# Performance work log

Hardware: AMD Instinct MI355X
Metric: run time of the kernel (lower is better)

The kernel has to match this reference:

```python
import jax, jax.numpy as jnp
import numpy as np

IN_DIM = 128
OUT_DIM = 128
GRID_SIZE = 10
SPLINE_ORDER = 3  # k
N_TOKENS = 65536
LN_EPS = 1e-5


def setup_inputs() -> dict:
    key = jax.random.key(0)
    k0, k1, k2 = jax.random.split(key, 3)
    x = jax.random.normal(k0, (N_TOKENS, IN_DIM), dtype=jnp.float32)
    # uniform extended grid on [-1, 1]: [in, grid_size + 2k + 1]
    h = 2.0 / GRID_SIZE
    g1d = jnp.arange(-SPLINE_ORDER, GRID_SIZE + SPLINE_ORDER + 1, dtype=jnp.float32) * h - 1.0
    grid = jnp.tile(g1d[None, :], (IN_DIM, 1))
    base_w = jax.random.normal(k1, (OUT_DIM, IN_DIM), dtype=jnp.float32) / np.float32(np.sqrt(IN_DIM))
    n_coeff = GRID_SIZE + SPLINE_ORDER  # basis functions per input dim
    spline_w = jax.random.normal(k2, (OUT_DIM, IN_DIM * n_coeff), dtype=jnp.float32) * np.float32(0.1 / np.sqrt(IN_DIM))
    gamma = jnp.ones((OUT_DIM,), dtype=jnp.float32)
    beta = jnp.zeros((OUT_DIM,), dtype=jnp.float32)
    return {"x": x, "grid": grid, "base_w": base_w, "spline_w": spline_w, "gamma": gamma, "beta": beta}


def _b_splines(x, grid, k=SPLINE_ORDER):
    # x: [N, in], grid: [in, G+2k+1] -> basis [N, in, G+k] via Cox-de Boor
    xe = x[:, :, None]
    b = ((xe >= grid[:, :-1]) & (xe < grid[:, 1:])).astype(x.dtype)  # order-0
    for p in range(1, k + 1):
        left = (xe - grid[:, : -(p + 1)]) / (grid[:, p:-1] - grid[:, : -(p + 1)]) * b[..., :-1]
        right = (grid[:, p + 1 :] - xe) / (grid[:, p + 1 :] - grid[:, 1:-p]) * b[..., 1:]
        b = left + right
    return b


def reference(x, grid, base_w, spline_w, gamma, beta):
    n = x.shape[0]
    basis = _b_splines(x, grid)  # [N, in, G+k]
    kan = jax.nn.silu(x) @ base_w.T + basis.reshape(n, -1) @ spline_w.T  # [N, out]
    # LayerNorm over last dim
    mu = jnp.mean(kan, axis=-1, keepdims=True)
    var = jnp.mean(jnp.square(kan - mu), axis=-1, keepdims=True)
    out = (kan - mu) * jax.lax.rsqrt(var + LN_EPS) * gamma + beta
    # dropout is identity in eval mode; skip = Identity since in_dim == out_dim
    return out + x
```

## Files before the change

kernel.cpp:

```cpp
#include <hip/hip_runtime.h>


#define DIM 128
#define NCOEFF 13
#define SLOT 16
#define KTOT (DIM * SLOT)
#define DPC 8
#define KC (DPC * SLOT)
#define NCHUNK (DIM / DPC)
#define MTILE 64
#define ABUF (MTILE * DPC * SLOT)
#define XSTR 68
#define WB_BYTES (DIM * KTOT * 2)

typedef __attribute__((ext_vector_type(8))) short short8;
typedef __attribute__((ext_vector_type(8))) __bf16 bf16x8;
typedef __attribute__((ext_vector_type(4))) float f32x4;
typedef __attribute__((ext_vector_type(2))) unsigned long long u64x2;

__device__ __forceinline__ unsigned short f2bf(float f) {
  unsigned int u = __builtin_bit_cast(unsigned int, f);
  u += 0x7fffu + ((u >> 16) & 1u);
  return (unsigned short)(u >> 16);
}

__global__ void kan_prep_wfrag(const float* __restrict__ base_w,
                               const float* __restrict__ spline_w,
                               unsigned short* __restrict__ Wf) {
  int u = blockIdx.x * 256 + threadIdx.x;
  int lane = u & 63;
  int blk = u >> 6;
  int ntile = blk & 7;
  int khi = blk >> 3;
  int q = lane >> 4, ln = lane & 15;
  int n = ntile * 16 + ln;
  int k0 = khi * 32 + q * 8;
  unsigned short v[8];
#pragma unroll
  for (int j = 0; j < 8; ++j) {
    int k = k0 + j;
    int i = k >> 4, s = k & 15;
    float f = (s == 0) ? base_w[n * DIM + i]
            : (s <= 13 ? spline_w[n * (DIM * NCOEFF) + i * NCOEFF + (s - 1)] : 0.f);
    v[j] = f2bf(f);
  }
  short8 pack;
#pragma unroll
  for (int j = 0; j < 8; ++j) pack[j] = (short)v[j];
  ((short8*)Wf)[u] = pack;
}

__device__ __forceinline__ void build_slots(float xv, unsigned long long r[4]) {
  float sil = xv * __builtin_amdgcn_rcpf(1.0f + __expf(-xv));
  float tp = (xv + 1.6f) * 5.0f;
  int m = (int)floorf(tp);
  bool valid = (xv >= -1.6f) && (xv < 1.6f);
  m = m < 0 ? 0 : (m > 15 ? 15 : m);
  float u = tp - (float)m;
  float omu = 1.0f - u;
  float w0 = 0.166666667f * omu * omu * omu;
  float w3 = 0.166666667f * u * u * u;
  float w1 = (0.5f * u - 1.0f) * u * u + 0.666666667f;
  float w2 = (0.5f * omu - 1.0f) * omu * omu + 0.666666667f;
  unsigned long long W =
      (unsigned long long)f2bf(w0) |
      ((unsigned long long)f2bf(w1) << 16) |
      ((unsigned long long)f2bf(w2) << 32) |
      ((unsigned long long)f2bf(w3) << 48);
  if (!valid) W = 0;
  int p = m - 2;
#pragma unroll
  for (int j = 0; j < 4; ++j) {
    int d = 64 * j - 16 * p;
    unsigned long long rj;
    if (d >= 64 || d <= -64) rj = 0;
    else if (d >= 0) rj = W >> d;
    else rj = W << (-d);
    r[j] = rj;
  }
  r[0] = (r[0] & ~0xFFFFULL) | (unsigned long long)f2bf(sil);
  r[3] &= 0xFFFFFFFFULL;
}

__device__ __forceinline__ int a_off(int t, int i, int h) {
  return (((i >> 1) * 4 + (t >> 4)) << 9) + ((((i & 1) * 2 + h) << 4) + (t & 15)) * 8;
}

__device__ __forceinline__ void stage_elem(unsigned short* Ab, int t, int i, float xv) {
  unsigned long long r[4];
  build_slots(xv, r);
  *(short8*)(Ab + a_off(t, i, 0)) = __builtin_bit_cast(short8, (u64x2){r[0], r[1]});
  *(short8*)(Ab + a_off(t, i, 1)) = __builtin_bit_cast(short8, (u64x2){r[2], r[3]});
}

template <bool BF16W>
__global__ __launch_bounds__(256, 4)
void kan_fused(const float* __restrict__ x,
               const unsigned short* __restrict__ Wf,
               const float* __restrict__ base_w,
               const float* __restrict__ spline_w,
               const float* __restrict__ gamma,
               const float* __restrict__ beta,
               float* __restrict__ out) {
  __shared__ __align__(16) unsigned short A_lds[2][ABUF];
  __shared__ float x_lds[2][DPC * XSTR];
  __shared__ float S1p[4][MTILE];
  __shared__ float S2p[4][MTILE];

  const int tid = threadIdx.x;
  const int lane = tid & 63, wave = tid >> 6;
  const int q = lane >> 4, ln = lane & 15;
  const long tokBase = (long)blockIdx.x * MTILE;

  f32x4 acc[4][2];
#pragma unroll
  for (int a = 0; a < 4; ++a)
#pragma unroll
    for (int b = 0; b < 2; ++b) acc[a][b] = (f32x4){0.f, 0.f, 0.f, 0.f};

  const int iw = tid & 7;
  const int t0 = tid >> 3;
  const int ts = tid & 63;
  const int i2 = tid >> 6;

  {
    float xa = x[(tokBase + ts) * DIM + i2];
    float xb = x[(tokBase + ts) * DIM + i2 + 4];
    stage_elem(A_lds[0], ts, i2, xa);
    stage_elem(A_lds[0], ts, i2 + 4, xb);
    float f0 = x[(tokBase + t0) * DIM + DPC + iw];
    float f1 = x[(tokBase + t0 + 32) * DIM + DPC + iw];
    x_lds[1][iw * XSTR + t0] = f0;
    x_lds[1][iw * XSTR + t0 + 32] = f1;
  }
  short8 bfr[4][2];
#pragma unroll
  for (int ks = 0; ks < 4; ++ks)
#pragma unroll
    for (int nt = 0; nt < 2; ++nt) {
      if (BF16W) {
        bfr[ks][nt] = *(const short8*)(Wf + ((ks * 8) + wave * 2 + nt) * 512 + lane * 8);
      } else {
        const int n = wave * 32 + nt * 16 + ln;
        const int kg = ks * 32 + q * 8;
        float f[8];
        int i = kg >> 4, s0 = kg & 15;
        if (s0 == 0) {
          f[0] = base_w[n * DIM + i];
#pragma unroll
          for (int j = 0; j < 7; ++j) f[1 + j] = spline_w[n * (DIM * NCOEFF) + i * NCOEFF + j];
        } else {
#pragma unroll
          for (int j = 0; j < 6; ++j) f[j] = spline_w[n * (DIM * NCOEFF) + i * NCOEFF + 7 + j];
          f[6] = 0.f; f[7] = 0.f;
        }
        short8 tmp;
#pragma unroll
        for (int j = 0; j < 8; ++j) tmp[j] = (short)f2bf(f[j]);
        bfr[ks][nt] = tmp;
      }
    }

  for (int c = 0; c < NCHUNK; ++c) {
    __syncthreads();
    float xg0 = 0.f, xg1 = 0.f;
    if (c + 2 < NCHUNK) {
      const float* xc = x + (c + 2) * DPC + iw;
      xg0 = xc[(tokBase + t0) * DIM];
      xg1 = xc[(tokBase + t0 + 32) * DIM];
    }
    const unsigned short* Ab = A_lds[c & 1];
#pragma unroll
    for (int ks = 0; ks < 4; ++ks) {
      short8 af[4];
#pragma unroll
      for (int mt = 0; mt < 4; ++mt)
        af[mt] = *(const short8*)&Ab[((ks * 4 + mt) << 9) + lane * 8];
#pragma unroll
      for (int mt = 0; mt < 4; ++mt)
#pragma unroll
        for (int nt = 0; nt < 2; ++nt)
          acc[mt][nt] = __builtin_amdgcn_mfma_f32_16x16x32_bf16(
              __builtin_bit_cast(bf16x8, af[mt]), __builtin_bit_cast(bf16x8, bfr[ks][nt]),
              acc[mt][nt], 0, 0, 0);
    }
    if (c + 1 < NCHUNK) {
#pragma unroll
      for (int ks = 0; ks < 4; ++ks)
#pragma unroll
        for (int nt = 0; nt < 2; ++nt) {
          if (BF16W) {
            bfr[ks][nt] = *(const short8*)(Wf + (((c + 1) * 4 + ks) * 8 + wave * 2 + nt) * 512 + lane * 8);
          } else {
            const int n = wave * 32 + nt * 16 + ln;
            const int kg = (c + 1) * KC + ks * 32 + q * 8;
            float f[8];
            int i = kg >> 4, s0 = kg & 15;
            if (s0 == 0) {
              f[0] = base_w[n * DIM + i];
#pragma unroll
              for (int j = 0; j < 7; ++j) f[1 + j] = spline_w[n * (DIM * NCOEFF) + i * NCOEFF + j];
            } else {
#pragma unroll
              for (int j = 0; j < 6; ++j) f[j] = spline_w[n * (DIM * NCOEFF) + i * NCOEFF + 7 + j];
              f[6] = 0.f; f[7] = 0.f;
            }
            short8 tmp;
#pragma unroll
            for (int j = 0; j < 8; ++j) tmp[j] = (short)f2bf(f[j]);
            bfr[ks][nt] = tmp;
          }
        }
      const float* xs = x_lds[(c + 1) & 1];
      unsigned short* Bb = A_lds[(c + 1) & 1];
      stage_elem(Bb, ts, i2, xs[i2 * XSTR + ts]);
      stage_elem(Bb, ts, i2 + 4, xs[(i2 + 4) * XSTR + ts]);
    }
    if (c + 2 < NCHUNK) {
      float* xd = x_lds[c & 1];
      xd[iw * XSTR + t0] = xg0;
      xd[iw * XSTR + t0 + 32] = xg1;
    }
  }

#pragma unroll
  for (int mt = 0; mt < 4; ++mt) {
#pragma unroll
    for (int r = 0; r < 4; ++r) {
      float s1 = 0.f, s2 = 0.f;
#pragma unroll
      for (int nt = 0; nt < 2; ++nt) { float v = acc[mt][nt][r]; s1 += v; s2 += v * v; }
#pragma unroll
      for (int off = 1; off < 16; off <<= 1) {
        s1 += __shfl_xor(s1, off);
        s2 += __shfl_xor(s2, off);
      }
      if (ln == 0) {
        int t = mt * 16 + q * 4 + r;
        S1p[wave][t] = s1;
        S2p[wave][t] = s2;
      }
    }
  }
  __syncthreads();
  float gv[2], bv[2];
#pragma unroll
  for (int nt = 0; nt < 2; ++nt) {
    int n = wave * 32 + nt * 16 + ln;
    gv[nt] = gamma[n];
    bv[nt] = beta[n];
  }
#pragma unroll
  for (int mt = 0; mt < 4; ++mt) {
#pragma unroll
    for (int r = 0; r < 4; ++r) {
      int t = mt * 16 + q * 4 + r;
      float s1 = S1p[0][t] + S1p[1][t] + S1p[2][t] + S1p[3][t];
      float s2 = S2p[0][t] + S2p[1][t] + S2p[2][t] + S2p[3][t];
      float mean = s1 * (1.0f / 128.0f);
      float var = s2 * (1.0f / 128.0f) - mean * mean;
      float inv = __builtin_amdgcn_rsqf(var + 1e-5f);
      long rowo = (tokBase + t) * DIM;
#pragma unroll
      for (int nt = 0; nt < 2; ++nt) {
        int n = wave * 32 + nt * 16 + ln;
        float o = (acc[mt][nt][r] - mean) * inv * gv[nt] + bv[nt] + x[rowo + n];
        out[rowo + n] = o;
      }
    }
  }
}

extern "C" void kernel_launch(void* const* d_in, const int* in_sizes, int n_in,
                              void* d_out, int out_size, void* d_ws, size_t ws_size,
                              hipStream_t stream) {
  const float* x        = (const float*)d_in[0];
  const float* base_w   = (const float*)d_in[2];
  const float* spline_w = (const float*)d_in[3];
  const float* gamma    = (const float*)d_in[4];
  const float* beta     = (const float*)d_in[5];
  float* out = (float*)d_out;

  const int n_tokens = in_sizes[0] / DIM;
  const int nblocks = n_tokens / MTILE;

  if (ws_size >= (size_t)WB_BYTES) {
    unsigned short* Wf = (unsigned short*)d_ws;
    kan_prep_wfrag<<<(DIM * KTOT / 8) / 256, 256, 0, stream>>>(base_w, spline_w, Wf);
    kan_fused<true><<<nblocks, 256, 0, stream>>>(x, Wf, base_w, spline_w, gamma, beta, out);
  } else {
    kan_fused<false><<<nblocks, 256, 0, stream>>>(x, nullptr, base_w, spline_w, gamma, beta, out);
  }
}
```

Before: 131.0 us.

## Halve token tile to 32 rows and truncate bf16 packing via perm

```diff
diff --git a/kernel.cpp b/kernel.cpp
--- a/kernel.cpp
+++ b/kernel.cpp
@@ -8,7 +8,7 @@
 #define DPC 8
 #define KC (DPC * SLOT)
 #define NCHUNK (DIM / DPC)
-#define MTILE 64
+#define MTILE 32
 #define ABUF (MTILE * DPC * SLOT)
 #define XSTR 68
 #define WB_BYTES (DIM * KTOT * 2)
@@ -62,11 +62,11 @@
   float w3 = 0.166666667f * u * u * u;
   float w1 = (0.5f * u - 1.0f) * u * u + 0.666666667f;
   float w2 = (0.5f * omu - 1.0f) * omu * omu + 0.666666667f;
-  unsigned long long W =
-      (unsigned long long)f2bf(w0) |
-      ((unsigned long long)f2bf(w1) << 16) |
-      ((unsigned long long)f2bf(w2) << 32) |
-      ((unsigned long long)f2bf(w3) << 48);
+  unsigned int lo = __builtin_amdgcn_perm(__builtin_bit_cast(unsigned int, w1),
+                                          __builtin_bit_cast(unsigned int, w0), 0x07060302u);
+  unsigned int hi = __builtin_amdgcn_perm(__builtin_bit_cast(unsigned int, w3),
+                                          __builtin_bit_cast(unsigned int, w2), 0x07060302u);
+  unsigned long long W = ((unsigned long long)hi << 32) | lo;
   if (!valid) W = 0;
   int p = m - 2;
 #pragma unroll
@@ -78,12 +78,13 @@
     else rj = W << (-d);
     r[j] = rj;
   }
-  r[0] = (r[0] & ~0xFFFFULL) | (unsigned long long)f2bf(sil);
+  unsigned int sb = __builtin_bit_cast(unsigned int, sil) >> 16;
+  r[0] = (r[0] & ~0xFFFFULL) | (unsigned long long)sb;
   r[3] &= 0xFFFFFFFFULL;
 }
 
 __device__ __forceinline__ int a_off(int t, int i, int h) {
-  return (((i >> 1) * 4 + (t >> 4)) << 9) + ((((i & 1) * 2 + h) << 4) + (t & 15)) * 8;
+  return (((i >> 1) * 2 + (t >> 4)) << 9) + ((((i & 1) * 2 + h) << 4) + (t & 15)) * 8;
 }
 
 __device__ __forceinline__ void stage_elem(unsigned short* Ab, int t, int i, float xv) {
@@ -94,7 +95,7 @@
 }
 
 template <bool BF16W>
-__global__ __launch_bounds__(256, 4)
+__global__ __launch_bounds__(256, 6)
 void kan_fused(const float* __restrict__ x,
                const unsigned short* __restrict__ Wf,
                const float* __restrict__ base_w,
@@ -112,26 +113,22 @@
   const int q = lane >> 4, ln = lane & 15;
   const long tokBase = (long)blockIdx.x * MTILE;
 
-  f32x4 acc[4][2];
-#pragma unroll
-  for (int a = 0; a < 4; ++a)
+  f32x4 acc[2][2];
+#pragma unroll
+  for (int a = 0; a < 2; ++a)
 #pragma unroll
     for (int b = 0; b < 2; ++b) acc[a][b] = (f32x4){0.f, 0.f, 0.f, 0.f};
 
   const int iw = tid & 7;
   const int t0 = tid >> 3;
-  const int ts = tid & 63;
-  const int i2 = tid >> 6;
+  const int ts = tid & 31;
+  const int i2 = tid >> 5;
 
   {
     float xa = x[(tokBase + ts) * DIM + i2];
-    float xb = x[(tokBase + ts) * DIM + i2 + 4];
     stage_elem(A_lds[0], ts, i2, xa);
-    stage_elem(A_lds[0], ts, i2 + 4, xb);
     float f0 = x[(tokBase + t0) * DIM + DPC + iw];
-    float f1 = x[(tokBase + t0 + 32) * DIM + DPC + iw];
     x_lds[1][iw * XSTR + t0] = f0;
-    x_lds[1][iw * XSTR + t0 + 32] = f1;
   }
   short8 bfr[4][2];
 #pragma unroll
@@ -139,7 +136,7 @@
 #pragma unroll
     for (int nt = 0; nt < 2; ++nt) {
       if (BF16W) {
-        bfr[ks][nt] = *(const short8*)(Wf + ((ks * 8) + wave * 2 + nt) * 512 + lane * 8);
+        bfr[ks][nt] = *(const short8*)(Wf + (ks * 8 + wave * 2 + nt) * 512 + lane * 8);
       } else {
         const int n = wave * 32 + nt * 16 + ln;
         const int kg = ks * 32 + q * 8;
@@ -163,21 +160,19 @@
 
   for (int c = 0; c < NCHUNK; ++c) {
     __syncthreads();
-    float xg0 = 0.f, xg1 = 0.f;
+    float xg0 = 0.f;
     if (c + 2 < NCHUNK) {
-      const float* xc = x + (c + 2) * DPC + iw;
-      xg0 = xc[(tokBase + t0) * DIM];
-      xg1 = xc[(tokBase + t0 + 32) * DIM];
+      xg0 = x[(tokBase + t0) * DIM + (c + 2) * DPC + iw];
     }
     const unsigned short* Ab = A_lds[c & 1];
 #pragma unroll
     for (int ks = 0; ks < 4; ++ks) {
-      short8 af[4];
-#pragma unroll
-      for (int mt = 0; mt < 4; ++mt)
-        af[mt] = *(const short8*)&Ab[((ks * 4 + mt) << 9) + lane * 8];
-#pragma unroll
-      for (int mt = 0; mt < 4; ++mt)
+      short8 af[2];
+#pragma unroll
+      for (int mt = 0; mt < 2; ++mt)
+        af[mt] = *(const short8*)&Ab[((ks * 2 + mt) << 9) + lane * 8];
+#pragma unroll
+      for (int mt = 0; mt < 2; ++mt)
 #pragma unroll
         for (int nt = 0; nt < 2; ++nt)
           acc[mt][nt] = __builtin_amdgcn_mfma_f32_16x16x32_bf16(
@@ -214,17 +209,14 @@
       const float* xs = x_lds[(c + 1) & 1];
       unsigned short* Bb = A_lds[(c + 1) & 1];
       stage_elem(Bb, ts, i2, xs[i2 * XSTR + ts]);
-      stage_elem(Bb, ts, i2 + 4, xs[(i2 + 4) * XSTR + ts]);
     }
     if (c + 2 < NCHUNK) {
-      float* xd = x_lds[c & 1];
-      xd[iw * XSTR + t0] = xg0;
-      xd[iw * XSTR + t0 + 32] = xg1;
-    }
-  }
-
-#pragma unroll
-  for (int mt = 0; mt < 4; ++mt) {
+      x_lds[c & 1][iw * XSTR + t0] = xg0;
+    }
+  }
+
+#pragma unroll
+  for (int mt = 0; mt < 2; ++mt) {
 #pragma unroll
     for (int r = 0; r < 4; ++r) {
       float s1 = 0.f, s2 = 0.f;
@@ -251,7 +243,7 @@
     bv[nt] = beta[n];
   }
 #pragma unroll
-  for (int mt = 0; mt < 4; ++mt) {
+  for (int mt = 0; mt < 2; ++mt) {
 #pragma unroll
     for (int r = 0; r < 4; ++r) {
       int t = mt * 16 + q * 4 + r;
```

Result: slower. 146.2 us (+11.6%).
